# Performance work log

Measured on AMD Instinct MI355X. Metric: run time of the kernel, lower is better.

The kernel has to match this reference:

```python
import jax, jax.numpy as jnp
import numpy as np

HIDDEN = 4096
HEADS = 32
HEAD_DIM = HIDDEN // HEADS  # 128; kv length must equal this (additive-bias broadcast)
B, SQ, SK = 4, 2048, HEAD_DIM


def _split_heads(x):
    # [B, T, HIDDEN] -> [B, H, T, d]
    b, t, _ = x.shape
    return x.reshape(b, t, HEADS, HEAD_DIM).transpose(0, 2, 1, 3)


def setup_inputs() -> dict:
    key = jax.random.key(0)
    ks = jax.random.split(key, 8)
    s = 1.0 / np.sqrt(HIDDEN)
    return {
        "q": jax.random.normal(ks[0], (B, SQ, HIDDEN), jnp.float32),
        "k": jax.random.normal(ks[1], (B, SK, HIDDEN), jnp.float32),
        "v": jax.random.normal(ks[2], (B, SK, HIDDEN), jnp.float32),
        "r": jax.random.normal(ks[3], (B, SQ, HIDDEN), jnp.float32),
        "Wq": jax.random.normal(ks[4], (HIDDEN, HIDDEN), jnp.float32) * s,
        "Wk": jax.random.normal(ks[5], (HIDDEN, HIDDEN), jnp.float32) * s,
        "Wv": jax.random.normal(ks[6], (HIDDEN, HIDDEN), jnp.float32) * s,
        "Wo": jax.random.normal(ks[7], (HIDDEN, HIDDEN), jnp.float32) * s,
    }


def reference(q, k, v, r, Wq, Wk, Wv, Wo):
    qh = _split_heads(q @ Wq)           # [B,H,SQ,d]
    kh = _split_heads(k @ Wk)           # [B,H,SK,d]
    vh = _split_heads(v @ Wv)           # [B,H,SK,d]
    rh = _split_heads(r @ Wo)           # [B,H,SQ,d] ; d == SK, added as bias
    scale = 1.0 / np.sqrt(HEAD_DIM).astype(np.float32)
    scores = jnp.einsum("bhqd,bhkd->bhqk", qh, kh) * scale + rh
    attn = jax.nn.softmax(scores, axis=-1)
    ctx = jnp.einsum("bhqk,bhkd->bhqd", attn, vh)       # [B,H,SQ,d]
    ctx = ctx.transpose(0, 2, 1, 3).reshape(q.shape[0], -1, HIDDEN)
    return ctx @ Wo  # Wo reused for output projection, as in source
```

## Files before the change

kernel.cpp:

```cpp
#include <hip/hip_runtime.h>
#include <hip/hip_bf16.h>

typedef unsigned short u16;
typedef unsigned int   u32;
typedef unsigned long long u64;
typedef __attribute__((ext_vector_type(8))) short short8;
typedef __attribute__((ext_vector_type(4))) float f32x4;

#define HID   4096
#define NHEAD 32
#define HD    128
#define NB    4
#define NSQ   2048
#define NSK   128
#define MROWS (NB*NSQ)
#define KROWS (NB*NSK)

__device__ __forceinline__ u16 f2bf(float f) {
  u32 u = __builtin_bit_cast(u32, f);
  u += 0x7fffu + ((u >> 16) & 1u);
  return (u16)(u >> 16);
}

__device__ __forceinline__ float bf2f(u16 x) {
  u32 u = (u32)x << 16;
  return __builtin_bit_cast(float, u);
}

__device__ __forceinline__ u64 pack4(float4 f) {
  return (u64)f2bf(f.x) | ((u64)f2bf(f.y) << 16) |
         ((u64)f2bf(f.z) << 32) | ((u64)f2bf(f.w) << 48);
}

__device__ __forceinline__ uint4 packu16x8(const u16* v) {
  uint4 o;
  o.x = (u32)v[0] | ((u32)v[1] << 16);
  o.y = (u32)v[2] | ((u32)v[3] << 16);
  o.z = (u32)v[4] | ((u32)v[5] << 16);
  o.w = (u32)v[6] | ((u32)v[7] << 16);
  return o;
}

__device__ __forceinline__ f32x4 mfma16(short8 a, short8 b, f32x4 c) {
  return __builtin_amdgcn_mfma_f32_16x16x32_bf16(a, b, c, 0, 0, 0);
}

__device__ __forceinline__ void gload_lds16(const u16* g, u16* l) {
  __builtin_amdgcn_global_load_lds((const __attribute__((address_space(1))) u32*)g,
                                   (__attribute__((address_space(3))) u32*)l, 16, 0, 0);
}

__global__ __launch_bounds__(256) void convert_bf16_x2(const float* __restrict__ in0,
                                                       u16* __restrict__ out0,
                                                       const float* __restrict__ in1,
                                                       u16* __restrict__ out1, long long n4)
{
  const float* in = blockIdx.y ? in1 : in0;
  u16* out = blockIdx.y ? out1 : out0;
  long long i = (long long)blockIdx.x * blockDim.x + threadIdx.x;
  const long long stride = (long long)gridDim.x * blockDim.x;
  for (; i < n4; i += stride) {
    float4 f = ((const float4*)in)[i];
    ((u64*)out)[i] = pack4(f);
  }
}

__global__ __launch_bounds__(256) void transpose_convert_x4(const float* __restrict__ W0, u16* __restrict__ T0,
                                                            const float* __restrict__ W1, u16* __restrict__ T1,
                                                            const float* __restrict__ W2, u16* __restrict__ T2,
                                                            const float* __restrict__ W3, u16* __restrict__ T3)
{
  const int z = blockIdx.z;
  const float* W = (z == 0) ? W0 : (z == 1) ? W1 : (z == 2) ? W2 : W3;
  u16* Wt = (z == 0) ? T0 : (z == 1) ? T1 : (z == 2) ? T2 : T3;
  __shared__ __align__(16) u16 tile[64][72];
  const int t = threadIdx.x;
  const int c0 = blockIdx.x * 64, r0 = blockIdx.y * 64;
  #pragma unroll
  for (int i = 0; i < 4; ++i) {
    int e = i * 1024 + t * 4;
    int rr = e >> 6, cc = e & 63;
    float4 f = *(const float4*)(W + (size_t)(r0 + rr) * HID + c0 + cc);
    *(u64*)&tile[rr][cc] = pack4(f);
  }
  __syncthreads();
  #pragma unroll
  for (int i = 0; i < 2; ++i) {
    int e = i * 2048 + t * 8;
    int cc = e >> 6, rr = e & 63;
    u16 vals[8];
    #pragma unroll
    for (int jj = 0; jj < 8; ++jj) vals[jj] = tile[rr + jj][cc];
    *(uint4*)(Wt + (size_t)(c0 + cc) * HID + r0 + rr) = packu16x8(vals);
  }
}

__global__ __launch_bounds__(256) void transpose_head(const u16* __restrict__ Vh,
                                                      u16* __restrict__ VT)
{
  __shared__ __align__(16) u16 tile[128][136];
  const int t = threadIdx.x;
  const int bh = blockIdx.x;
  const int b = bh >> 5, h = bh & 31;
  #pragma unroll
  for (int i = 0; i < 8; ++i) {
    int e = i * 2048 + t * 8;
    int tr = e >> 7, d = e & 127;
    *(uint4*)&tile[tr][d] = *(const uint4*)(Vh + ((size_t)b * NSK + tr) * HID + h * HD + d);
  }
  __syncthreads();
  #pragma unroll
  for (int i = 0; i < 8; ++i) {
    int e = i * 2048 + t * 8;
    int d = e >> 7, tt = e & 127;
    u16 vals[8];
    #pragma unroll
    for (int jj = 0; jj < 8; ++jj) vals[jj] = tile[tt + jj][d];
    *(uint4*)(VT + ((size_t)bh * HD + d) * NSK + tt) = packu16x8(vals);
  }
}


__device__ __forceinline__ short8 ldf(const u16* buf, int r, int cb) {
  return *(const short8*)(buf + r * 64 + (cb ^ ((r & 7) << 3)));
}

__device__ __forceinline__ void stage2(u16* dst, const u16* g, long off0, long off1, int tid) {
  gload_lds16(g + off0, dst + tid * 8);
  gload_lds16(g + off1, dst + 4096 + tid * 8);
}

template<int VM, bool S1, bool S2>
__device__ __forceinline__ void tile4(const u16* __restrict__ Ag, const u16* __restrict__ Bg,
                                      int kt, u16* Ac, u16* Bc, u16* Ao, u16* Bo,
                                      int wm, int wn, int g, int c16,
                                      long off0, long off1, int tid, f32x4 (&acc)[8][4])
{
  const int g8 = g * 8;
  short8 af[4][2], bf[4][2];

  #pragma unroll
  for (int i = 0; i < 4; ++i) {
    const int r = wm * 128 + i * 16 + c16;
    af[i][0] = ldf(Ac, r, g8); af[i][1] = ldf(Ac, r, 32 + g8);
  }
  #pragma unroll
  for (int j = 0; j < 2; ++j) {
    const int r = wn * 64 + j * 16 + c16;
    bf[j][0] = ldf(Bc, r, g8); bf[j][1] = ldf(Bc, r, 32 + g8);
  }
  if constexpr (S1) stage2(Ao + 8192, Ag + (size_t)128 * HID + kt + 64, off0, off1, tid);
  asm volatile("s_waitcnt lgkmcnt(8)" ::: "memory");
  __builtin_amdgcn_s_barrier();
  asm volatile("s_waitcnt lgkmcnt(0)" ::: "memory");
  __builtin_amdgcn_sched_barrier(0);
  __builtin_amdgcn_s_setprio(1);
  #pragma unroll
  for (int i = 0; i < 4; ++i)
    #pragma unroll
    for (int j = 0; j < 2; ++j) {
      acc[i][j] = mfma16(af[i][0], bf[j][0], acc[i][j]);
      acc[i][j] = mfma16(af[i][1], bf[j][1], acc[i][j]);
    }
  __builtin_amdgcn_s_setprio(0);

  #pragma unroll
  for (int j = 2; j < 4; ++j) {
    const int r = wn * 64 + j * 16 + c16;
    bf[j][0] = ldf(Bc, r, g8); bf[j][1] = ldf(Bc, r, 32 + g8);
  }
  if constexpr (S1) stage2(Bo + 8192, Bg + (size_t)128 * HID + kt + 64, off0, off1, tid);
  __builtin_amdgcn_s_barrier();
  asm volatile("s_waitcnt lgkmcnt(0)" ::: "memory");
  __builtin_amdgcn_sched_barrier(0);
  __builtin_amdgcn_s_setprio(1);
  #pragma unroll
  for (int i = 0; i < 4; ++i)
    #pragma unroll
    for (int j = 2; j < 4; ++j) {
      acc[i][j] = mfma16(af[i][0], bf[j][0], acc[i][j]);
      acc[i][j] = mfma16(af[i][1], bf[j][1], acc[i][j]);
    }
  __builtin_amdgcn_s_setprio(0);

  #pragma unroll
  for (int i = 0; i < 4; ++i) {
    const int r = wm * 128 + 64 + i * 16 + c16;
    af[i][0] = ldf(Ac, r, g8); af[i][1] = ldf(Ac, r, 32 + g8);
  }
  if constexpr (S2) stage2(Bc, Bg + kt + 128, off0, off1, tid);
  __builtin_amdgcn_s_barrier();
  asm volatile("s_waitcnt lgkmcnt(0)" ::: "memory");
  __builtin_amdgcn_sched_barrier(0);
  __builtin_amdgcn_s_setprio(1);
  #pragma unroll
  for (int i = 0; i < 4; ++i)
    #pragma unroll
    for (int j = 0; j < 2; ++j) {
      acc[4 + i][j] = mfma16(af[i][0], bf[j][0], acc[4 + i][j]);
      acc[4 + i][j] = mfma16(af[i][1], bf[j][1], acc[4 + i][j]);
    }
  __builtin_amdgcn_s_setprio(0);

  if constexpr (S2) stage2(Ac, Ag + kt + 128, off0, off1, tid);
  if constexpr (VM == 4) {
    asm volatile("s_waitcnt vmcnt(4)" ::: "memory");
  } else if constexpr (VM == 0) {
    asm volatile("s_waitcnt vmcnt(0)" ::: "memory");
  }
  __builtin_amdgcn_s_barrier();
  __builtin_amdgcn_sched_barrier(0);
  __builtin_amdgcn_s_setprio(1);
  #pragma unroll
  for (int i = 0; i < 4; ++i)
    #pragma unroll
    for (int j = 2; j < 4; ++j) {
      acc[4 + i][j] = mfma16(af[i][0], bf[j][0], acc[4 + i][j]);
      acc[4 + i][j] = mfma16(af[i][1], bf[j][1], acc[4 + i][j]);
    }
  __builtin_amdgcn_s_setprio(0);
}

template<bool OUTF32>
__device__ __forceinline__ void gemm_body(const u16* __restrict__ Ag,
                                          const u16* __restrict__ Bg,
                                          u16* __restrict__ Ch, float* __restrict__ Cf,
                                          int n0, int tid,
                                          u16* As0, u16* As1, u16* Bs0, u16* Bs1)
{
  const int l = tid & 63, wv = tid >> 6;
  const int g = l >> 4 & 3, c16 = l & 15;
  const int wm = wv >> 2, wn = wv & 3;

  const long off0 = (long)(tid >> 3) * HID + (((tid & 7) ^ ((tid >> 3) & 7)) * 8);
  const long off1 = off0 + (long)64 * HID;

  f32x4 acc[8][4] = {};

  stage2(Bs0,        Bg,                     off0, off1, tid);
  stage2(As0,        Ag,                     off0, off1, tid);
  stage2(As0 + 8192, Ag + (size_t)128 * HID, off0, off1, tid);
  stage2(Bs0 + 8192, Bg + (size_t)128 * HID, off0, off1, tid);
  stage2(Bs1,        Bg + 64,                off0, off1, tid);
  stage2(As1,        Ag + 64,                off0, off1, tid);
  asm volatile("s_waitcnt vmcnt(4)" ::: "memory");
  __builtin_amdgcn_sched_barrier(0);
  __builtin_amdgcn_s_barrier();

  constexpr int NT = HID / 64;
  for (int T = 0; T < NT - 3; T += 2) {
    tile4<4, true, true>(Ag, Bg, T * 64,      As0, Bs0, As1, Bs1,
                         wm, wn, g, c16, off0, off1, tid, acc);
    tile4<4, true, true>(Ag, Bg, T * 64 + 64, As1, Bs1, As0, Bs0,
                         wm, wn, g, c16, off0, off1, tid, acc);
  }
  tile4<0, true, false>(Ag, Bg, (NT - 2) * 64, As0, Bs0, As1, Bs1,
                        wm, wn, g, c16, off0, off1, tid, acc);
  tile4<-1, false, false>(Ag, Bg, (NT - 1) * 64, As1, Bs1, As0, Bs0,
                          wm, wn, g, c16, off0, off1, tid, acc);

  #pragma unroll
  for (int mi = 0; mi < 8; ++mi)
    #pragma unroll
    for (int j = 0; j < 4; ++j)
      #pragma unroll
      for (int rr = 0; rr < 4; ++rr) {
        const size_t idx = (size_t)(wm * 128 + mi * 16 + g * 4 + rr) * HID
                         + n0 + wn * 64 + j * 16 + c16;
        if constexpr (OUTF32) Cf[idx] = acc[mi][j][rr];
        else                  Ch[idx] = f2bf(acc[mi][j][rr]);
      }
}

__global__ __launch_bounds__(512, 2) void gemm_mega(const u16* __restrict__ qb,
                                                    const u16* __restrict__ WqT,
                                                    u16* __restrict__ Qh,
                                                    const u16* __restrict__ rb,
                                                    const u16* __restrict__ WoT,
                                                    u16* __restrict__ Rhb,
                                                    const u16* __restrict__ kvb,
                                                    const u16* __restrict__ WkT,
                                                    const u16* __restrict__ WvT,
                                                    u16* __restrict__ Kh,
                                                    u16* __restrict__ Vh,
                                                    int nQ, int nR)
{
  __shared__ __align__(16) u16 As[2][16384];
  __shared__ __align__(16) u16 Bs[2][16384];
  const int tid = threadIdx.x;

  const int nwg = gridDim.x;
  int wg = blockIdx.x;
  wg = (wg & 7) * (nwg >> 3) + (wg >> 3);

  const u16* Ag; const u16* Bg; u16* Ch; int n0;
  if (wg < nQ) {
    const int m0 = (wg >> 4) * 256; n0 = (wg & 15) * 256;
    Ag = qb + (size_t)m0 * HID;  Bg = WqT + (size_t)n0 * HID;  Ch = Qh + (size_t)m0 * HID;
  } else if (wg < nQ + nR) {
    const int e = wg - nQ;
    const int m0 = (e >> 4) * 256; n0 = (e & 15) * 256;
    Ag = rb + (size_t)m0 * HID;  Bg = WoT + (size_t)n0 * HID;  Ch = Rhb + (size_t)m0 * HID;
  } else {
    const int e = wg - nQ - nR, mt = e >> 4;
    n0 = (e & 15) * 256;
    Ag = kvb + (size_t)(mt << 8) * HID;
    Bg = (mt < 2 ? WkT : WvT) + (size_t)n0 * HID;
    Ch = (mt < 2 ? Kh : Vh) + (size_t)((mt & 1) << 8) * HID;
  }

  gemm_body<false>(Ag, Bg, Ch, nullptr, n0, tid, &As[0][0], &As[1][0], &Bs[0][0], &Bs[1][0]);
}

__global__ __launch_bounds__(512, 2) void gemm256f(const u16* __restrict__ A,
                                                   const u16* __restrict__ Bt,
                                                   float* __restrict__ C)
{
  __shared__ __align__(16) u16 As[2][16384];
  __shared__ __align__(16) u16 Bs[2][16384];
  const int tid = threadIdx.x;

  const int nwg = gridDim.x;
  int wg = blockIdx.x;
  wg = (wg & 7) * (nwg >> 3) + (wg >> 3);
  const int m0 = (wg >> 4) * 256, n0 = (wg & 15) * 256;

  gemm_body<true>(A + (size_t)m0 * HID, Bt + (size_t)n0 * HID,
                  nullptr, C + (size_t)m0 * HID, n0, tid,
                  &As[0][0], &As[1][0], &Bs[0][0], &Bs[1][0]);
}

__global__ __launch_bounds__(256) void attn_kernel(const u16*  __restrict__ Qh,
                                                   const u16*  __restrict__ Kh,
                                                   const u16*  __restrict__ VT,
                                                   const u16*  __restrict__ Rhb,
                                                   u16* __restrict__ ctx)
{
  __shared__ __align__(16) u16 Plds[4][32][136];
  const int t = threadIdx.x;
  const int w = t >> 6, l = t & 63;
  const int g = l >> 4, c = l & 15;
  const int qc = blockIdx.x;
  const int bh = blockIdx.y;
  const int b = bh >> 5, h = bh & 31;
  const size_t qrow0 = (size_t)b * NSQ + qc * 128 + w * 32;
  const float SCALE = 0.08838834764831845f;

  f32x4 s[2][8] = {};
  #pragma unroll
  for (int ks = 0; ks < 4; ++ks) {
    const int ko = ks * 32 + g * 8;
    short8 af[2];
    #pragma unroll
    for (int i = 0; i < 2; ++i)
      af[i] = *(const short8*)(Qh + (qrow0 + i * 16 + c) * HID + h * HD + ko);
    #pragma unroll
    for (int j = 0; j < 8; ++j) {
      short8 bfr = *(const short8*)(Kh + ((size_t)b * NSK + j * 16 + c) * HID + h * HD + ko);
      s[0][j] = mfma16(af[0], bfr, s[0][j]);
      s[1][j] = mfma16(af[1], bfr, s[1][j]);
    }
  }

  float rinv[2][4];
  #pragma unroll
  for (int i = 0; i < 2; ++i) {
    #pragma unroll
    for (int rr = 0; rr < 4; ++rr) {
      const size_t qr = qrow0 + i * 16 + g * 4 + rr;
      float vmax = -3.0e38f;
      #pragma unroll
      for (int j = 0; j < 8; ++j) {
        float bias = bf2f(Rhb[qr * HID + h * HD + j * 16 + c]);
        float sv = s[i][j][rr] * SCALE + bias;
        s[i][j][rr] = sv;
        vmax = fmaxf(vmax, sv);
      }
      #pragma unroll
      for (int m = 1; m < 16; m <<= 1) vmax = fmaxf(vmax, __shfl_xor(vmax, m));
      float ssum = 0.f;
      #pragma unroll
      for (int j = 0; j < 8; ++j) {
        float p = __expf(s[i][j][rr] - vmax);
        s[i][j][rr] = p;
        ssum += p;
      }
      #pragma unroll
      for (int m = 1; m < 16; m <<= 1) ssum += __shfl_xor(ssum, m);
      rinv[i][rr] = 1.f / ssum;
    }
  }

  #pragma unroll
  for (int i = 0; i < 2; ++i)
    #pragma unroll
    for (int j = 0; j < 8; ++j)
      #pragma unroll
      for (int rr = 0; rr < 4; ++rr)
        Plds[w][i * 16 + g * 4 + rr][j * 16 + c] = f2bf(s[i][j][rr]);
  __syncthreads();

  #pragma unroll
  for (int i = 0; i < 2; ++i) {
    f32x4 o[8] = {};
    #pragma unroll
    for (int ks = 0; ks < 4; ++ks) {
      const int ko = ks * 32 + g * 8;
      short8 pa = *(const short8*)(&Plds[w][i * 16 + c][ko]);
      #pragma unroll
      for (int j = 0; j < 8; ++j) {
        short8 bv = *(const short8*)(VT + ((size_t)bh * HD + j * 16 + c) * NSK + ko);
        o[j] = mfma16(pa, bv, o[j]);
      }
    }
    #pragma unroll
    for (int j = 0; j < 8; ++j)
      #pragma unroll
      for (int rr = 0; rr < 4; ++rr) {
        const size_t row = qrow0 + i * 16 + g * 4 + rr;
        ctx[row * HID + h * HD + j * 16 + c] = f2bf(o[j][rr] * rinv[i][rr]);
      }
  }
}

extern "C" void kernel_launch(void* const* d_in, const int* in_sizes, int n_in,
                              void* d_out, int out_size, void* d_ws, size_t ws_size,
                              hipStream_t stream)
{
  const float* q  = (const float*)d_in[0];
  const float* k  = (const float*)d_in[1];
  const float* v  = (const float*)d_in[2];
  const float* r  = (const float*)d_in[3];
  const float* Wq = (const float*)d_in[4];
  const float* Wk = (const float*)d_in[5];
  const float* Wv = (const float*)d_in[6];
  const float* Wo = (const float*)d_in[7];
  float* out = (float*)d_out;

  char* ws = (char*)d_ws;
  #define WSMB(x) ((size_t)(x) << 20)
  u16* WoT = (u16*)(ws + WSMB(0));
  u16* Qh  = (u16*)(ws + WSMB(32));
  u16* Kh  = (u16*)(ws + WSMB(96));
  u16* Vh  = (u16*)(ws + WSMB(100));
  u16* VTb = (u16*)(ws + WSMB(104));
  u16* rb  = (u16*)(ws + WSMB(108));
  u16* ctx = (u16*)(ws + WSMB(108));
  u16* Sb  = (u16*)(ws + WSMB(172));
  u16* WqT = (u16*)(ws + WSMB(236));
  if (ws_size < WSMB(268)) return;
  const bool wide = (ws_size >= WSMB(276));

  dim3 tb(256);
  dim3 tb5(512);
  const long long nBig = (long long)MROWS * HID / 4;
  const long long nSm  = (long long)KROWS * HID / 4;

  if (wide) {
    u16* Rhb = (u16*)((char*)d_out + WSMB(0));
    u16* WkT = (u16*)((char*)d_out + WSMB(64));
    u16* WvT = (u16*)((char*)d_out + WSMB(96));
    u16* kvb = (u16*)(ws + WSMB(268));
    u16* vbp = kvb + (size_t)KROWS * HID;

    transpose_convert_x4<<<dim3(64, 64, 4), tb, 0, stream>>>(Wo, WoT, Wq, WqT, Wk, WkT, Wv, WvT);
    convert_bf16_x2<<<dim3(512, 2), tb, 0, stream>>>(k, kvb, v, vbp, nSm);
    convert_bf16_x2<<<dim3(2048, 2), tb, 0, stream>>>(q, Sb, r, rb, nBig);

    gemm_mega<<<dim3(1088), tb5, 0, stream>>>(Sb, WqT, Qh, rb, WoT, Rhb,
                                              kvb, WkT, WvT, Kh, Vh, 512, 512);

    transpose_head<<<dim3(128), tb, 0, stream>>>(Vh, VTb);
    attn_kernel<<<dim3(16, 128), tb, 0, stream>>>(Qh, Kh, VTb, Rhb, ctx);
    gemm256f<<<dim3(512), tb5, 0, stream>>>(ctx, WoT, out);
  } else {
    u16* WkT = (u16*)((char*)d_out + WSMB(0));
    u16* WvT = (u16*)((char*)d_out + WSMB(32));
    u16* kvb = (u16*)((char*)d_out + WSMB(64));
    u16* vbp = kvb + (size_t)KROWS * HID;

    transpose_convert_x4<<<dim3(64, 64, 4), tb, 0, stream>>>(Wo, WoT, Wq, WqT, Wk, WkT, Wv, WvT);
    convert_bf16_x2<<<dim3(512, 2), tb, 0, stream>>>(k, kvb, v, vbp, nSm);
    convert_bf16_x2<<<dim3(2048, 2), tb, 0, stream>>>(q, Sb, r, rb, nBig);

    gemm_mega<<<dim3(576), tb5, 0, stream>>>(Sb, WqT, Qh, nullptr, nullptr, nullptr,
                                             kvb, WkT, WvT, Kh, Vh, 512, 0);
    gemm_mega<<<dim3(512), tb5, 0, stream>>>(nullptr, nullptr, nullptr, rb, WoT, Sb,
                                             nullptr, nullptr, nullptr, nullptr, nullptr, 0, 512);

    transpose_head<<<dim3(128), tb, 0, stream>>>(Vh, VTb);
    attn_kernel<<<dim3(16, 128), tb, 0, stream>>>(Qh, Kh, VTb, Sb, ctx);
    gemm256f<<<dim3(512), tb5, 0, stream>>>(ctx, WoT, out);
  }
}
```

Baseline: 1.125 ms.

## Restructure GEMM k-tile into two phases, stage bias in LDS, drop wide path

The GEMM inner tile goes from four barrier-separated MFMA phases to two. All B fragments are loaded up front and both next-tile stages are issued together, which cuts barriers per k-tile but raises register pressure and shifts when the prefetches land. The attention kernel now loads its additive-bias tile into shared memory with coalesced 16-byte loads before the QK MFMAs, instead of doing strided scalar global reads, and reuses that buffer for P. The launcher also drops the wide-workspace fused-launch path and always runs the two-launch projection sequence.

```diff
diff --git a/kernel.cpp b/kernel.cpp
--- a/kernel.cpp
+++ b/kernel.cpp
@@ -131,7 +131,7 @@
 }
 
 template<int VM, bool S1, bool S2>
-__device__ __forceinline__ void tile4(const u16* __restrict__ Ag, const u16* __restrict__ Bg,
+__device__ __forceinline__ void tile2(const u16* __restrict__ Ag, const u16* __restrict__ Bg,
                                       int kt, u16* Ac, u16* Bc, u16* Ao, u16* Bo,
                                       int wm, int wn, int g, int c16,
                                       long off0, long off1, int tid, f32x4 (&acc)[8][4])
@@ -145,11 +145,14 @@
     af[i][0] = ldf(Ac, r, g8); af[i][1] = ldf(Ac, r, 32 + g8);
   }
   #pragma unroll
-  for (int j = 0; j < 2; ++j) {
+  for (int j = 0; j < 4; ++j) {
     const int r = wn * 64 + j * 16 + c16;
     bf[j][0] = ldf(Bc, r, g8); bf[j][1] = ldf(Bc, r, 32 + g8);
   }
-  if constexpr (S1) stage2(Ao + 8192, Ag + (size_t)128 * HID + kt + 64, off0, off1, tid);
+  if constexpr (S1) {
+    stage2(Ao + 8192, Ag + (size_t)128 * HID + kt + 64, off0, off1, tid);
+    stage2(Bo + 8192, Bg + (size_t)128 * HID + kt + 64, off0, off1, tid);
+  }
   asm volatile("s_waitcnt lgkmcnt(8)" ::: "memory");
   __builtin_amdgcn_s_barrier();
   asm volatile("s_waitcnt lgkmcnt(0)" ::: "memory");
@@ -158,18 +161,29 @@
   #pragma unroll
   for (int i = 0; i < 4; ++i)
     #pragma unroll
-    for (int j = 0; j < 2; ++j) {
+    for (int j = 0; j < 4; ++j)
       acc[i][j] = mfma16(af[i][0], bf[j][0], acc[i][j]);
+  #pragma unroll
+  for (int i = 0; i < 4; ++i)
+    #pragma unroll
+    for (int j = 0; j < 4; ++j)
       acc[i][j] = mfma16(af[i][1], bf[j][1], acc[i][j]);
-    }
   __builtin_amdgcn_s_setprio(0);
 
   #pragma unroll
-  for (int j = 2; j < 4; ++j) {
-    const int r = wn * 64 + j * 16 + c16;
-    bf[j][0] = ldf(Bc, r, g8); bf[j][1] = ldf(Bc, r, 32 + g8);
-  }
-  if constexpr (S1) stage2(Bo + 8192, Bg + (size_t)128 * HID + kt + 64, off0, off1, tid);
+  for (int i = 0; i < 4; ++i) {
+    const int r = wm * 128 + 64 + i * 16 + c16;
+    af[i][0] = ldf(Ac, r, g8); af[i][1] = ldf(Ac, r, 32 + g8);
+  }
+  if constexpr (S2) {
+    stage2(Bc, Bg + kt + 128, off0, off1, tid);
+    stage2(Ac, Ag + kt + 128, off0, off1, tid);
+  }
+  if constexpr (VM == 4) {
+    asm volatile("s_waitcnt vmcnt(4)" ::: "memory");
+  } else if constexpr (VM == 0) {
+    asm volatile("s_waitcnt vmcnt(0)" ::: "memory");
+  }
   __builtin_amdgcn_s_barrier();
   asm volatile("s_waitcnt lgkmcnt(0)" ::: "memory");
   __builtin_amdgcn_sched_barrier(0);
@@ -177,47 +191,13 @@
   #pragma unroll
   for (int i = 0; i < 4; ++i)
     #pragma unroll
-    for (int j = 2; j < 4; ++j) {
-      acc[i][j] = mfma16(af[i][0], bf[j][0], acc[i][j]);
-      acc[i][j] = mfma16(af[i][1], bf[j][1], acc[i][j]);
-    }
-  __builtin_amdgcn_s_setprio(0);
-
-  #pragma unroll
-  for (int i = 0; i < 4; ++i) {
-    const int r = wm * 128 + 64 + i * 16 + c16;
-    af[i][0] = ldf(Ac, r, g8); af[i][1] = ldf(Ac, r, 32 + g8);
-  }
-  if constexpr (S2) stage2(Bc, Bg + kt + 128, off0, off1, tid);
-  __builtin_amdgcn_s_barrier();
-  asm volatile("s_waitcnt lgkmcnt(0)" ::: "memory");
-  __builtin_amdgcn_sched_barrier(0);
-  __builtin_amdgcn_s_setprio(1);
+    for (int j = 0; j < 4; ++j)
+      acc[4 + i][j] = mfma16(af[i][0], bf[j][0], acc[4 + i][j]);
   #pragma unroll
   for (int i = 0; i < 4; ++i)
     #pragma unroll
-    for (int j = 0; j < 2; ++j) {
-      acc[4 + i][j] = mfma16(af[i][0], bf[j][0], acc[4 + i][j]);
+    for (int j = 0; j < 4; ++j)
       acc[4 + i][j] = mfma16(af[i][1], bf[j][1], acc[4 + i][j]);
-    }
-  __builtin_amdgcn_s_setprio(0);
-
-  if constexpr (S2) stage2(Ac, Ag + kt + 128, off0, off1, tid);
-  if constexpr (VM == 4) {
-    asm volatile("s_waitcnt vmcnt(4)" ::: "memory");
-  } else if constexpr (VM == 0) {
-    asm volatile("s_waitcnt vmcnt(0)" ::: "memory");
-  }
-  __builtin_amdgcn_s_barrier();
-  __builtin_amdgcn_sched_barrier(0);
-  __builtin_amdgcn_s_setprio(1);
-  #pragma unroll
-  for (int i = 0; i < 4; ++i)
-    #pragma unroll
-    for (int j = 2; j < 4; ++j) {
-      acc[4 + i][j] = mfma16(af[i][0], bf[j][0], acc[4 + i][j]);
-      acc[4 + i][j] = mfma16(af[i][1], bf[j][1], acc[4 + i][j]);
-    }
   __builtin_amdgcn_s_setprio(0);
 }
 
@@ -249,14 +229,14 @@
 
   constexpr int NT = HID / 64;
   for (int T = 0; T < NT - 3; T += 2) {
-    tile4<4, true, true>(Ag, Bg, T * 64,      As0, Bs0, As1, Bs1,
+    tile2<4, true, true>(Ag, Bg, T * 64,      As0, Bs0, As1, Bs1,
                          wm, wn, g, c16, off0, off1, tid, acc);
-    tile4<4, true, true>(Ag, Bg, T * 64 + 64, As1, Bs1, As0, Bs0,
+    tile2<4, true, true>(Ag, Bg, T * 64 + 64, As1, Bs1, As0, Bs0,
                          wm, wn, g, c16, off0, off1, tid, acc);
   }
-  tile4<0, true, false>(Ag, Bg, (NT - 2) * 64, As0, Bs0, As1, Bs1,
+  tile2<0, true, false>(Ag, Bg, (NT - 2) * 64, As0, Bs0, As1, Bs1,
                         wm, wn, g, c16, off0, off1, tid, acc);
-  tile4<-1, false, false>(Ag, Bg, (NT - 1) * 64, As1, Bs1, As0, Bs0,
+  tile2<-1, false, false>(Ag, Bg, (NT - 1) * 64, As1, Bs1, As0, Bs0,
                           wm, wn, g, c16, off0, off1, tid, acc);
 
   #pragma unroll
@@ -336,7 +316,7 @@
                                                    const u16*  __restrict__ Rhb,
                                                    u16* __restrict__ ctx)
 {
-  __shared__ __align__(16) u16 Plds[4][32][136];
+  __shared__ __align__(16) u16 sh[4][32][136];
   const int t = threadIdx.x;
   const int w = t >> 6, l = t & 63;
   const int g = l >> 4, c = l & 15;
@@ -346,6 +326,14 @@
   const size_t qrow0 = (size_t)b * NSQ + qc * 128 + w * 32;
   const float SCALE = 0.08838834764831845f;
 
+  const u16* brow = Rhb + ((size_t)b * NSQ + qc * 128) * HID + h * HD;
+  #pragma unroll
+  for (int it = 0; it < 8; ++it) {
+    int e = it * 2048 + t * 8;
+    int rr_ = e >> 7, cc = e & 127;
+    *(uint4*)&sh[rr_ >> 5][rr_ & 31][cc] = *(const uint4*)(brow + (size_t)rr_ * HID + cc);
+  }
+
   f32x4 s[2][8] = {};
   #pragma unroll
   for (int ks = 0; ks < 4; ++ks) {
@@ -361,17 +349,18 @@
       s[1][j] = mfma16(af[1], bfr, s[1][j]);
     }
   }
+  __syncthreads();
 
   float rinv[2][4];
   #pragma unroll
   for (int i = 0; i < 2; ++i) {
     #pragma unroll
     for (int rr = 0; rr < 4; ++rr) {
-      const size_t qr = qrow0 + i * 16 + g * 4 + rr;
+      const int lr = i * 16 + g * 4 + rr;
       float vmax = -3.0e38f;
       #pragma unroll
       for (int j = 0; j < 8; ++j) {
-        float bias = bf2f(Rhb[qr * HID + h * HD + j * 16 + c]);
+        float bias = bf2f(sh[w][lr][j * 16 + c]);
         float sv = s[i][j][rr] * SCALE + bias;
         s[i][j][rr] = sv;
         vmax = fmaxf(vmax, sv);
@@ -397,7 +386,7 @@
     for (int j = 0; j < 8; ++j)
       #pragma unroll
       for (int rr = 0; rr < 4; ++rr)
-        Plds[w][i * 16 + g * 4 + rr][j * 16 + c] = f2bf(s[i][j][rr]);
+        sh[w][i * 16 + g * 4 + rr][j * 16 + c] = f2bf(s[i][j][rr]);
   __syncthreads();
 
   #pragma unroll
@@ -406,7 +395,7 @@
     #pragma unroll
     for (int ks = 0; ks < 4; ++ks) {
       const int ko = ks * 32 + g * 8;
-      short8 pa = *(const short8*)(&Plds[w][i * 16 + c][ko]);
+      short8 pa = *(const short8*)(&sh[w][i * 16 + c][ko]);
       #pragma unroll
       for (int j = 0; j < 8; ++j) {
         short8 bv = *(const short8*)(VT + ((size_t)bh * HD + j * 16 + c) * NSK + ko);
@@ -448,48 +437,30 @@
   u16* ctx = (u16*)(ws + WSMB(108));
   u16* Sb  = (u16*)(ws + WSMB(172));
   u16* WqT = (u16*)(ws + WSMB(236));
-  if (ws_size < WSMB(268)) return;
-  const bool wide = (ws_size >= WSMB(276));
+  u16* WkT = (u16*)((char*)d_out + WSMB(0));
+  u16* WvT = (u16*)((char*)d_out + WSMB(32));
+  u16* kvb = (u16*)((char*)d_out + WSMB(64));
+  u16* vbp = kvb + (size_t)KROWS * HID;
+  const size_t needed = WSMB(268);
+  if (ws_size < needed) return;
 
   dim3 tb(256);
   dim3 tb5(512);
   const long long nBig = (long long)MROWS * HID / 4;
   const long long nSm  = (long long)KROWS * HID / 4;
 
-  if (wide) {
-    u16* Rhb = (u16*)((char*)d_out + WSMB(0));
-    u16* WkT = (u16*)((char*)d_out + WSMB(64));
-    u16* WvT = (u16*)((char*)d_out + WSMB(96));
-    u16* kvb = (u16*)(ws + WSMB(268));
-    u16* vbp = kvb + (size_t)KROWS * HID;
-
-    transpose_convert_x4<<<dim3(64, 64, 4), tb, 0, stream>>>(Wo, WoT, Wq, WqT, Wk, WkT, Wv, WvT);
-    convert_bf16_x2<<<dim3(512, 2), tb, 0, stream>>>(k, kvb, v, vbp, nSm);
-    convert_bf16_x2<<<dim3(2048, 2), tb, 0, stream>>>(q, Sb, r, rb, nBig);
-
-    gemm_mega<<<dim3(1088), tb5, 0, stream>>>(Sb, WqT, Qh, rb, WoT, Rhb,
-                                              kvb, WkT, WvT, Kh, Vh, 512, 512);
-
-    transpose_head<<<dim3(128), tb, 0, stream>>>(Vh, VTb);
-    attn_kernel<<<dim3(16, 128), tb, 0, stream>>>(Qh, Kh, VTb, Rhb, ctx);
-    gemm256f<<<dim3(512), tb5, 0, stream>>>(ctx, WoT, out);
-  } else {
-    u16* WkT = (u16*)((char*)d_out + WSMB(0));
-    u16* WvT = (u16*)((char*)d_out + WSMB(32));
-    u16* kvb = (u16*)((char*)d_out + WSMB(64));
-    u16* vbp = kvb + (size_t)KROWS * HID;
-
-    transpose_convert_x4<<<dim3(64, 64, 4), tb, 0, stream>>>(Wo, WoT, Wq, WqT, Wk, WkT, Wv, WvT);
-    convert_bf16_x2<<<dim3(512, 2), tb, 0, stream>>>(k, kvb, v, vbp, nSm);
-    convert_bf16_x2<<<dim3(2048, 2), tb, 0, stream>>>(q, Sb, r, rb, nBig);
-
-    gemm_mega<<<dim3(576), tb5, 0, stream>>>(Sb, WqT, Qh, nullptr, nullptr, nullptr,
-                                             kvb, WkT, WvT, Kh, Vh, 512, 0);
-    gemm_mega<<<dim3(512), tb5, 0, stream>>>(nullptr, nullptr, nullptr, rb, WoT, Sb,
-                                             nullptr, nullptr, nullptr, nullptr, nullptr, 0, 512);
-
-    transpose_head<<<dim3(128), tb, 0, stream>>>(Vh, VTb);
-    attn_kernel<<<dim3(16, 128), tb, 0, stream>>>(Qh, Kh, VTb, Sb, ctx);
-    gemm256f<<<dim3(512), tb5, 0, stream>>>(ctx, WoT, out);
-  }
-}
+  transpose_convert_x4<<<dim3(64, 64, 4), tb, 0, stream>>>(Wo, WoT, Wq, WqT, Wk, WkT, Wv, WvT);
+  convert_bf16_x2<<<dim3(512, 2), tb, 0, stream>>>(k, kvb, v, vbp, nSm);
+  convert_bf16_x2<<<dim3(2048, 2), tb, 0, stream>>>(q, Sb, r, rb, nBig);
+
+  gemm_mega<<<dim3(576), tb5, 0, stream>>>(Sb, WqT, Qh, nullptr, nullptr, nullptr,
+                                           kvb, WkT, WvT, Kh, Vh, 512, 0);
+  gemm_mega<<<dim3(512), tb5, 0, stream>>>(nullptr, nullptr, nullptr, rb, WoT, Sb,
+                                           nullptr, nullptr, nullptr, nullptr, nullptr, 0, 512);
+
+  transpose_head<<<dim3(128), tb, 0, stream>>>(Vh, VTb);
+
+  attn_kernel<<<dim3(16, 128), tb, 0, stream>>>(Qh, Kh, VTb, Sb, ctx);
+
+  gemm256f<<<dim3(512), tb5, 0, stream>>>(ctx, WoT, out);
+}
```

After: 0.9998 ms (median of 3 runs). 11.1% less time.
